# Performance work log

Hardware: AMD Instinct MI355X
Metric: run time of the kernel (lower is better)

The kernel has to match this reference:

```python
import jax, jax.numpy as jnp
import numpy as np

B, C, T, H, NCLS = 512, 22, 1000, 64, 4


def setup_inputs() -> dict:
    key = jax.random.key(0)
    ks = jax.random.split(key, 8)
    s_ih = 1.0 / np.sqrt(H)
    x = jax.random.normal(ks[0], (B, C, T), dtype=jnp.float32)
    # PyTorch LSTM params: gate order [i, f, g, o], each of size H
    W_ih = jax.random.uniform(ks[1], (4 * H, C), minval=-s_ih, maxval=s_ih, dtype=jnp.float32)
    W_hh = jax.random.uniform(ks[2], (4 * H, H), minval=-s_ih, maxval=s_ih, dtype=jnp.float32)
    b_ih = jax.random.uniform(ks[3], (4 * H,), minval=-s_ih, maxval=s_ih, dtype=jnp.float32)
    b_hh = jax.random.uniform(ks[4], (4 * H,), minval=-s_ih, maxval=s_ih, dtype=jnp.float32)
    s_fc = 1.0 / np.sqrt(H * T)
    W_fc = jax.random.uniform(ks[5], (NCLS, H * T), minval=-s_fc, maxval=s_fc, dtype=jnp.float32)
    b_fc = jax.random.uniform(ks[6], (NCLS,), minval=-s_fc, maxval=s_fc, dtype=jnp.float32)
    return {"x": x, "W_ih": W_ih, "W_hh": W_hh, "b_ih": b_ih, "b_hh": b_hh,
            "W_fc": W_fc, "b_fc": b_fc}


def _lstm(xs, W_ih, W_hh, b_ih, b_hh):
    # xs: [B, T, C] -> outputs [B, T, H]
    b = xs.shape[0]
    # precompute input projections for all timesteps: [T, B, 4H]
    x_proj = jnp.einsum('btc,gc->tbg', xs, W_ih) + (b_ih + b_hh)
    h0 = jnp.zeros((b, W_hh.shape[1]), xs.dtype)
    c0 = jnp.zeros_like(h0)

    def step(carry, xp):
        h, c = carry
        gates = xp + h @ W_hh.T  # [B, 4H]
        i, f, g, o = jnp.split(gates, 4, axis=-1)
        i = jax.nn.sigmoid(i)
        f = jax.nn.sigmoid(f)
        g = jnp.tanh(g)
        o = jax.nn.sigmoid(o)
        c = f * c + i * g
        h = o * jnp.tanh(c)
        return (h, c), h

    _, hs = jax.lax.scan(step, (h0, c0), x_proj)  # hs: [T, B, H]
    return jnp.transpose(hs, (1, 0, 2))  # [B, T, H]


def reference(x, W_ih, W_hh, b_ih, b_hh, W_fc, b_fc):
    xs = jnp.transpose(x, (0, 2, 1))  # [B, T, C]  (permute(0,2,1))
    hs = _lstm(xs, W_ih, W_hh, b_ih, b_hh)  # [B, T, H]
    flat = hs.reshape(hs.shape[0], -1)  # [B, T*H], time-major per row
    logits = flat @ W_fc.T + b_fc  # [B, 4]
    return jax.nn.softmax(logits, axis=1)
```

## Files before the change

### kernel.cpp

```cpp
#include <hip/hip_runtime.h>

#define BB   512
#define CC   22
#define TT   1000
#define HH   64
#define NCLS 4
#define TC   250
#define NCHUNK (TT / TC)
#define XROW 12

typedef _Float16 f16;
typedef __attribute__((ext_vector_type(2))) _Float16 h2;

__device__ __forceinline__ float sigm(float x) {
    return 1.0f / (1.0f + __expf(-x));
}
__device__ __forceinline__ float tanh_(float x) {
    float e = __expf(-2.0f * fabsf(x));
    float r = (1.0f - e) / (1.0f + e);
    return copysignf(r, x);
}

__device__ __forceinline__ h2 u2h(unsigned u) {
    union { unsigned u; h2 h; } c; c.u = u; return c.h;
}
__device__ __forceinline__ unsigned h2u(h2 h) {
    union { unsigned u; h2 h; } c; c.h = h; return c.u;
}

__global__ __launch_bounds__(64, 1) void lstm_wave(
    const float* __restrict__ x,
    const float* __restrict__ W_ih,
    const float* __restrict__ W_hh,
    const float* __restrict__ b_ih,
    const float* __restrict__ b_hh,
    const float* __restrict__ W_fc,
    const float* __restrict__ b_fc,
    float* __restrict__ out)
{
    __shared__ __align__(16) h2  xs[TC][XROW];
    __shared__ __align__(16) f16 hbuf[HH];

    const int lane = threadIdx.x;
    const int r    = blockIdx.x;

    unsigned whh[4][32];
    unsigned wih[4][11];
    float bias[4];
    #pragma unroll
    for (int g = 0; g < 4; ++g) {
        const int row = g * HH + lane;
        const float* wr = W_hh + row * HH;
        #pragma unroll
        for (int k = 0; k < 32; ++k)
            whh[g][k] = h2u(h2{(f16)wr[2 * k], (f16)wr[2 * k + 1]});
        const float* wi = W_ih + row * CC;
        #pragma unroll
        for (int k = 0; k < 11; ++k)
            wih[g][k] = h2u(h2{(f16)wi[2 * k], (f16)wi[2 * k + 1]});
        bias[g] = b_ih[row] + b_hh[row];
    }
    #pragma unroll
    for (int g = 0; g < 4; ++g) {
        #pragma unroll
        for (int k = 0; k < 32; ++k) asm volatile("" : "+v"(whh[g][k]));
        #pragma unroll
        for (int k = 0; k < 11; ++k) asm volatile("" : "+v"(wih[g][k]));
        asm volatile("" : "+v"(bias[g]));
    }

    hbuf[lane] = (f16)0.0f;
    float c = 0.0f;
    float fc0 = 0.f, fc1 = 0.f, fc2 = 0.f, fc3 = 0.f;
    const float* p0 = W_fc + 0 * (TT * HH) + lane;
    const float* p1 = W_fc + 1 * (TT * HH) + lane;
    const float* p2 = W_fc + 2 * (TT * HH) + lane;
    const float* p3 = W_fc + 3 * (TT * HH) + lane;
    const float* xrow = x + (size_t)r * (CC * TT);

    for (int chunk = 0; chunk < NCHUNK; ++chunk) {
        for (int tb = 0; tb < TC; tb += 64) {
            const int t = tb + lane;
            if (t < TC) {
                const float* gx = xrow + chunk * TC + t;
                union { h2 h[XROW]; uint4 q[3]; } U;
                #pragma unroll
                for (int k = 0; k < 11; ++k)
                    U.h[k] = h2{(f16)gx[(2 * k) * TT], (f16)gx[(2 * k + 1) * TT]};
                U.h[11] = h2{(f16)0.0f, (f16)0.0f};
                uint4* dst = (uint4*)&xs[t][0];
                dst[0] = U.q[0]; dst[1] = U.q[1]; dst[2] = U.q[2];
            }
        }

        for (int tt = 0; tt < TC; ++tt) {
            union { uint4 q[8]; h2 h[32]; } H;
            const uint4* hr = (const uint4*)hbuf;
            #pragma unroll
            for (int i = 0; i < 8; ++i) H.q[i] = hr[i];

            union { uint4 q[3]; h2 h[XROW]; } X;
            const uint4* xr = (const uint4*)&xs[tt][0];
            X.q[0] = xr[0]; X.q[1] = xr[1]; X.q[2] = xr[2];

            float w0 = *p0, w1 = *p1, w2 = *p2, w3 = *p3;
            p0 += HH; p1 += HH; p2 += HH; p3 += HH;

            float a0 = bias[0], a1 = bias[1], a2 = bias[2], a3 = bias[3];
            #pragma unroll
            for (int k = 0; k < 11; ++k) {
                a0 = __builtin_amdgcn_fdot2(X.h[k], u2h(wih[0][k]), a0, false);
                a1 = __builtin_amdgcn_fdot2(X.h[k], u2h(wih[1][k]), a1, false);
                a2 = __builtin_amdgcn_fdot2(X.h[k], u2h(wih[2][k]), a2, false);
                a3 = __builtin_amdgcn_fdot2(X.h[k], u2h(wih[3][k]), a3, false);
            }
            #pragma unroll
            for (int k = 0; k < 32; ++k) {
                a0 = __builtin_amdgcn_fdot2(H.h[k], u2h(whh[0][k]), a0, false);
                a1 = __builtin_amdgcn_fdot2(H.h[k], u2h(whh[1][k]), a1, false);
                a2 = __builtin_amdgcn_fdot2(H.h[k], u2h(whh[2][k]), a2, false);
                a3 = __builtin_amdgcn_fdot2(H.h[k], u2h(whh[3][k]), a3, false);
            }

            float iv = sigm(a0), fv = sigm(a1), gv = tanh_(a2), ov = sigm(a3);
            c = fv * c + iv * gv;
            float h = ov * tanh_(c);

            fc0 += h * w0; fc1 += h * w1; fc2 += h * w2; fc3 += h * w3;

            hbuf[lane] = (f16)h;
        }
    }

    #pragma unroll
    for (int off = 32; off; off >>= 1) {
        fc0 += __shfl_down(fc0, off);
        fc1 += __shfl_down(fc1, off);
        fc2 += __shfl_down(fc2, off);
        fc3 += __shfl_down(fc3, off);
    }
    if (lane == 0) {
        float l0 = fc0 + b_fc[0], l1 = fc1 + b_fc[1];
        float l2 = fc2 + b_fc[2], l3 = fc3 + b_fc[3];
        float m  = fmaxf(fmaxf(l0, l1), fmaxf(l2, l3));
        float e0 = __expf(l0 - m), e1 = __expf(l1 - m);
        float e2 = __expf(l2 - m), e3 = __expf(l3 - m);
        float s  = e0 + e1 + e2 + e3;
        float4 o; o.x = e0 / s; o.y = e1 / s; o.z = e2 / s; o.w = e3 / s;
        *(float4*)(out + r * NCLS) = o;
    }
}

extern "C" void kernel_launch(void* const* d_in, const int* in_sizes, int n_in,
                              void* d_out, int out_size, void* d_ws, size_t ws_size,
                              hipStream_t stream) {
    const float* x    = (const float*)d_in[0];
    const float* W_ih = (const float*)d_in[1];
    const float* W_hh = (const float*)d_in[2];
    const float* b_ih = (const float*)d_in[3];
    const float* b_hh = (const float*)d_in[4];
    const float* W_fc = (const float*)d_in[5];
    const float* b_fc = (const float*)d_in[6];
    float* out = (float*)d_out;

    lstm_wave<<<BB, 64, 0, stream>>>(x, W_ih, W_hh, b_ih, b_hh, W_fc, b_fc, out);
}
```

Baseline: 681.1 us.

## Split LSTM gate dot products across two waves with per-step LDS reduction

Each block now runs two waves. Each wave holds half of the recurrent and input weight columns and computes partial gate sums over its half of h and x. The partial sums are swapped through a double-buffered shared array with a barrier every timestep, which roughly halves the serial fdot2 chain per step. The price is a workgroup barrier and an LDS round trip inside the recurrence. Divisions in sigmoid, tanh and softmax are also replaced with hardware reciprocal approximations.

```diff
diff --git a/kernel.cpp b/kernel.cpp
--- a/kernel.cpp
+++ b/kernel.cpp
@@ -7,17 +7,18 @@
 #define NCLS 4
 #define TC   250
 #define NCHUNK (TT / TC)
-#define XROW 12
+#define XSL  16
 
 typedef _Float16 f16;
 typedef __attribute__((ext_vector_type(2))) _Float16 h2;
 
 __device__ __forceinline__ float sigm(float x) {
-    return 1.0f / (1.0f + __expf(-x));
+    float e = __expf(-x);
+    return __builtin_amdgcn_rcpf(1.0f + e);
 }
 __device__ __forceinline__ float tanh_(float x) {
     float e = __expf(-2.0f * fabsf(x));
-    float r = (1.0f - e) / (1.0f + e);
+    float r = (1.0f - e) * __builtin_amdgcn_rcpf(1.0f + e);
     return copysignf(r, x);
 }
 
@@ -28,7 +29,7 @@
     union { unsigned u; h2 h; } c; c.h = h; return c.u;
 }
 
-__global__ __launch_bounds__(64, 1) void lstm_wave(
+__global__ __launch_bounds__(128, 1) void lstm_wave2(
     const float* __restrict__ x,
     const float* __restrict__ W_ih,
     const float* __restrict__ W_hh,
@@ -38,95 +39,120 @@
     const float* __restrict__ b_fc,
     float* __restrict__ out)
 {
-    __shared__ __align__(16) h2  xs[TC][XROW];
-    __shared__ __align__(16) f16 hbuf[HH];
+    __shared__ __align__(16) h2    xs[TC][XSL];
+    __shared__ __align__(16) f16   hbuf[HH];
+    __shared__ __align__(16) float part[2][2][HH][4];
+    __shared__ float tmp4[NCLS];
 
-    const int lane = threadIdx.x;
+    const int tid  = threadIdx.x;
+    const int w    = tid >> 6;
+    const int lane = tid & 63;
     const int r    = blockIdx.x;
 
-    unsigned whh[4][32];
-    unsigned wih[4][11];
-    float bias[4];
+    unsigned whh[4][16];
+    unsigned wih[4][6];
+    float    bias[4];
     #pragma unroll
     for (int g = 0; g < 4; ++g) {
         const int row = g * HH + lane;
-        const float* wr = W_hh + row * HH;
+        const float* wr = W_hh + row * HH + 32 * w;
         #pragma unroll
-        for (int k = 0; k < 32; ++k)
+        for (int k = 0; k < 16; ++k)
             whh[g][k] = h2u(h2{(f16)wr[2 * k], (f16)wr[2 * k + 1]});
-        const float* wi = W_ih + row * CC;
+        const float* wi = W_ih + row * CC + 12 * w;
         #pragma unroll
-        for (int k = 0; k < 11; ++k)
-            wih[g][k] = h2u(h2{(f16)wi[2 * k], (f16)wi[2 * k + 1]});
-        bias[g] = b_ih[row] + b_hh[row];
+        for (int k = 0; k < 6; ++k) {
+            unsigned v = 0u;
+            if (w == 0 || k < 5)
+                v = h2u(h2{(f16)wi[2 * k], (f16)wi[2 * k + 1]});
+            wih[g][k] = v;
+        }
+        bias[g] = (w == 0) ? (b_ih[row] + b_hh[row]) : 0.0f;
     }
     #pragma unroll
     for (int g = 0; g < 4; ++g) {
         #pragma unroll
-        for (int k = 0; k < 32; ++k) asm volatile("" : "+v"(whh[g][k]));
+        for (int k = 0; k < 16; ++k) asm volatile("" : "+v"(whh[g][k]));
         #pragma unroll
-        for (int k = 0; k < 11; ++k) asm volatile("" : "+v"(wih[g][k]));
+        for (int k = 0; k < 6; ++k)  asm volatile("" : "+v"(wih[g][k]));
         asm volatile("" : "+v"(bias[g]));
     }
 
     hbuf[lane] = (f16)0.0f;
     float c = 0.0f;
-    float fc0 = 0.f, fc1 = 0.f, fc2 = 0.f, fc3 = 0.f;
-    const float* p0 = W_fc + 0 * (TT * HH) + lane;
-    const float* p1 = W_fc + 1 * (TT * HH) + lane;
-    const float* p2 = W_fc + 2 * (TT * HH) + lane;
-    const float* p3 = W_fc + 3 * (TT * HH) + lane;
+    float fca = 0.0f, fcb = 0.0f;
+    const float* pa = W_fc + (size_t)(2 * w)     * (TT * HH) + lane;
+    const float* pb = W_fc + (size_t)(2 * w + 1) * (TT * HH) + lane;
     const float* xrow = x + (size_t)r * (CC * TT);
 
     for (int chunk = 0; chunk < NCHUNK; ++chunk) {
-        for (int tb = 0; tb < TC; tb += 64) {
-            const int t = tb + lane;
+        for (int tb = 0; tb < TC; tb += 128) {
+            const int t = tb + tid;
             if (t < TC) {
                 const float* gx = xrow + chunk * TC + t;
-                union { h2 h[XROW]; uint4 q[3]; } U;
+                union { h2 h[XSL]; uint4 q[4]; } U;
                 #pragma unroll
-                for (int k = 0; k < 11; ++k)
+                for (int k = 0; k < 6; ++k)
                     U.h[k] = h2{(f16)gx[(2 * k) * TT], (f16)gx[(2 * k + 1) * TT]};
-                U.h[11] = h2{(f16)0.0f, (f16)0.0f};
+                U.h[6] = h2{(f16)0.0f, (f16)0.0f};
+                U.h[7] = h2{(f16)0.0f, (f16)0.0f};
+                #pragma unroll
+                for (int j = 0; j < 5; ++j)
+                    U.h[8 + j] = h2{(f16)gx[(12 + 2 * j) * TT], (f16)gx[(13 + 2 * j) * TT]};
+                U.h[13] = h2{(f16)0.0f, (f16)0.0f};
+                U.h[14] = h2{(f16)0.0f, (f16)0.0f};
+                U.h[15] = h2{(f16)0.0f, (f16)0.0f};
                 uint4* dst = (uint4*)&xs[t][0];
-                dst[0] = U.q[0]; dst[1] = U.q[1]; dst[2] = U.q[2];
+                dst[0] = U.q[0]; dst[1] = U.q[1]; dst[2] = U.q[2]; dst[3] = U.q[3];
             }
         }
+        __syncthreads();
 
         for (int tt = 0; tt < TC; ++tt) {
-            union { uint4 q[8]; h2 h[32]; } H;
-            const uint4* hr = (const uint4*)hbuf;
+            float wa = *pa, wb = *pb;
+            pa += HH; pb += HH;
+
+            union { uint4 q[4]; h2 h[16]; } H;
+            const uint4* hr = (const uint4*)(hbuf + 32 * w);
             #pragma unroll
-            for (int i = 0; i < 8; ++i) H.q[i] = hr[i];
+            for (int i = 0; i < 4; ++i) H.q[i] = hr[i];
 
-            union { uint4 q[3]; h2 h[XROW]; } X;
-            const uint4* xr = (const uint4*)&xs[tt][0];
-            X.q[0] = xr[0]; X.q[1] = xr[1]; X.q[2] = xr[2];
-
-            float w0 = *p0, w1 = *p1, w2 = *p2, w3 = *p3;
-            p0 += HH; p1 += HH; p2 += HH; p3 += HH;
+            __align__(16) h2 X[6];
+            {
+                const h2* xp = &xs[tt][8 * w];
+                *(uint4*)&X[0] = *(const uint4*)xp;
+                *(uint2*)&X[4] = *(const uint2*)(xp + 4);
+            }
 
             float a0 = bias[0], a1 = bias[1], a2 = bias[2], a3 = bias[3];
             #pragma unroll
-            for (int k = 0; k < 11; ++k) {
-                a0 = __builtin_amdgcn_fdot2(X.h[k], u2h(wih[0][k]), a0, false);
-                a1 = __builtin_amdgcn_fdot2(X.h[k], u2h(wih[1][k]), a1, false);
-                a2 = __builtin_amdgcn_fdot2(X.h[k], u2h(wih[2][k]), a2, false);
-                a3 = __builtin_amdgcn_fdot2(X.h[k], u2h(wih[3][k]), a3, false);
+            for (int k = 0; k < 6; ++k) {
+                a0 = __builtin_amdgcn_fdot2(X[k], u2h(wih[0][k]), a0, false);
+                a1 = __builtin_amdgcn_fdot2(X[k], u2h(wih[1][k]), a1, false);
+                a2 = __builtin_amdgcn_fdot2(X[k], u2h(wih[2][k]), a2, false);
+                a3 = __builtin_amdgcn_fdot2(X[k], u2h(wih[3][k]), a3, false);
             }
             #pragma unroll
-            for (int k = 0; k < 32; ++k) {
+            for (int k = 0; k < 16; ++k) {
                 a0 = __builtin_amdgcn_fdot2(H.h[k], u2h(whh[0][k]), a0, false);
                 a1 = __builtin_amdgcn_fdot2(H.h[k], u2h(whh[1][k]), a1, false);
                 a2 = __builtin_amdgcn_fdot2(H.h[k], u2h(whh[2][k]), a2, false);
                 a3 = __builtin_amdgcn_fdot2(H.h[k], u2h(whh[3][k]), a3, false);
             }
 
+            const int buf = tt & 1;
+            float4 mine; mine.x = a0; mine.y = a1; mine.z = a2; mine.w = a3;
+            *(float4*)&part[buf][w][lane][0] = mine;
+            __syncthreads();
+            float4 oth = *(const float4*)&part[buf][1 - w][lane][0];
+            a0 += oth.x; a1 += oth.y; a2 += oth.z; a3 += oth.w;
+
             float iv = sigm(a0), fv = sigm(a1), gv = tanh_(a2), ov = sigm(a3);
             c = fv * c + iv * gv;
             float h = ov * tanh_(c);
 
-            fc0 += h * w0; fc1 += h * w1; fc2 += h * w2; fc3 += h * w3;
+            fca += h * wa;
+            fcb += h * wb;
 
             hbuf[lane] = (f16)h;
         }
@@ -134,19 +160,21 @@
 
     #pragma unroll
     for (int off = 32; off; off >>= 1) {
-        fc0 += __shfl_down(fc0, off);
-        fc1 += __shfl_down(fc1, off);
-        fc2 += __shfl_down(fc2, off);
-        fc3 += __shfl_down(fc3, off);
+        fca += __shfl_down(fca, off);
+        fcb += __shfl_down(fcb, off);
     }
     if (lane == 0) {
-        float l0 = fc0 + b_fc[0], l1 = fc1 + b_fc[1];
-        float l2 = fc2 + b_fc[2], l3 = fc3 + b_fc[3];
+        tmp4[2 * w]     = fca + b_fc[2 * w];
+        tmp4[2 * w + 1] = fcb + b_fc[2 * w + 1];
+    }
+    __syncthreads();
+    if (tid == 0) {
+        float l0 = tmp4[0], l1 = tmp4[1], l2 = tmp4[2], l3 = tmp4[3];
         float m  = fmaxf(fmaxf(l0, l1), fmaxf(l2, l3));
         float e0 = __expf(l0 - m), e1 = __expf(l1 - m);
         float e2 = __expf(l2 - m), e3 = __expf(l3 - m);
-        float s  = e0 + e1 + e2 + e3;
-        float4 o; o.x = e0 / s; o.y = e1 / s; o.z = e2 / s; o.w = e3 / s;
+        float is = __builtin_amdgcn_rcpf(e0 + e1 + e2 + e3);
+        float4 o; o.x = e0 * is; o.y = e1 * is; o.z = e2 * is; o.w = e3 * is;
         *(float4*)(out + r * NCLS) = o;
     }
 }
@@ -163,5 +191,5 @@
     const float* b_fc = (const float*)d_in[6];
     float* out = (float*)d_out;
 
-    lstm_wave<<<BB, 64, 0, stream>>>(x, W_ih, W_hh, b_ih, b_hh, W_fc, b_fc, out);
+    lstm_wave2<<<BB, 128, 0, stream>>>(x, W_ih, W_hh, b_ih, b_hh, W_fc, b_fc, out);
 }
```

Measured after the change: 708.9 us. +4.1%, slower.

## Process two batch rows per wave sharing register weights; use rcp for activations

Applied to the files above, without the earlier changes.

Each single-wave block now runs the LSTM recurrence for two batch rows, reusing the register-resident weight fragments and the per-step W_fc loads, and halving the grid. The two independent recurrences give instruction-level parallelism to hide LDS and transcendental latency. Divisions in sigmoid, tanh and softmax are replaced by hardware reciprocal approximations. The trade-off is fewer waves across the GPU, so the per-wave serial work doubles while CU-level parallelism drops.

```diff
diff --git a/kernel.cpp b/kernel.cpp
--- a/kernel.cpp
+++ b/kernel.cpp
@@ -13,11 +13,12 @@
 typedef __attribute__((ext_vector_type(2))) _Float16 h2;
 
 __device__ __forceinline__ float sigm(float x) {
-    return 1.0f / (1.0f + __expf(-x));
+    float e = __expf(-x);
+    return __builtin_amdgcn_rcpf(1.0f + e);
 }
 __device__ __forceinline__ float tanh_(float x) {
     float e = __expf(-2.0f * fabsf(x));
-    float r = (1.0f - e) / (1.0f + e);
+    float r = (1.0f - e) * __builtin_amdgcn_rcpf(1.0f + e);
     return copysignf(r, x);
 }
 
@@ -28,7 +29,7 @@
     union { unsigned u; h2 h; } c; c.h = h; return c.u;
 }
 
-__global__ __launch_bounds__(64, 1) void lstm_wave(
+__global__ __launch_bounds__(64, 1) void lstm_2row(
     const float* __restrict__ x,
     const float* __restrict__ W_ih,
     const float* __restrict__ W_hh,
@@ -38,11 +39,14 @@
     const float* __restrict__ b_fc,
     float* __restrict__ out)
 {
-    __shared__ __align__(16) h2  xs[TC][XROW];
-    __shared__ __align__(16) f16 hbuf[HH];
+    __shared__ __align__(16) h2  xsA[TC][XROW];
+    __shared__ __align__(16) h2  xsB[TC][XROW];
+    __shared__ __align__(16) f16 hbA[HH];
+    __shared__ __align__(16) f16 hbB[HH];
 
     const int lane = threadIdx.x;
-    const int r    = blockIdx.x;
+    const int rA   = blockIdx.x * 2;
+    const int rB   = rA + 1;
 
     unsigned whh[4][32];
     unsigned wih[4][11];
@@ -69,85 +73,123 @@
         asm volatile("" : "+v"(bias[g]));
     }
 
-    hbuf[lane] = (f16)0.0f;
-    float c = 0.0f;
-    float fc0 = 0.f, fc1 = 0.f, fc2 = 0.f, fc3 = 0.f;
+    hbA[lane] = (f16)0.0f;
+    hbB[lane] = (f16)0.0f;
+    float cA = 0.0f, cB = 0.0f;
+    float fa0 = 0.f, fa1 = 0.f, fa2 = 0.f, fa3 = 0.f;
+    float fb0 = 0.f, fb1 = 0.f, fb2 = 0.f, fb3 = 0.f;
     const float* p0 = W_fc + 0 * (TT * HH) + lane;
     const float* p1 = W_fc + 1 * (TT * HH) + lane;
     const float* p2 = W_fc + 2 * (TT * HH) + lane;
     const float* p3 = W_fc + 3 * (TT * HH) + lane;
-    const float* xrow = x + (size_t)r * (CC * TT);
+    const float* xrowA = x + (size_t)rA * (CC * TT);
+    const float* xrowB = x + (size_t)rB * (CC * TT);
 
     for (int chunk = 0; chunk < NCHUNK; ++chunk) {
         for (int tb = 0; tb < TC; tb += 64) {
             const int t = tb + lane;
             if (t < TC) {
-                const float* gx = xrow + chunk * TC + t;
-                union { h2 h[XROW]; uint4 q[3]; } U;
+                const float* gA = xrowA + chunk * TC + t;
+                const float* gB = xrowB + chunk * TC + t;
+                union { h2 h[XROW]; uint4 q[3]; } UA, UB;
                 #pragma unroll
-                for (int k = 0; k < 11; ++k)
-                    U.h[k] = h2{(f16)gx[(2 * k) * TT], (f16)gx[(2 * k + 1) * TT]};
-                U.h[11] = h2{(f16)0.0f, (f16)0.0f};
-                uint4* dst = (uint4*)&xs[t][0];
-                dst[0] = U.q[0]; dst[1] = U.q[1]; dst[2] = U.q[2];
+                for (int k = 0; k < 11; ++k) {
+                    UA.h[k] = h2{(f16)gA[(2 * k) * TT], (f16)gA[(2 * k + 1) * TT]};
+                    UB.h[k] = h2{(f16)gB[(2 * k) * TT], (f16)gB[(2 * k + 1) * TT]};
+                }
+                UA.h[11] = h2{(f16)0.0f, (f16)0.0f};
+                UB.h[11] = h2{(f16)0.0f, (f16)0.0f};
+                uint4* dA = (uint4*)&xsA[t][0];
+                uint4* dB = (uint4*)&xsB[t][0];
+                dA[0] = UA.q[0]; dA[1] = UA.q[1]; dA[2] = UA.q[2];
+                dB[0] = UB.q[0]; dB[1] = UB.q[1]; dB[2] = UB.q[2];
             }
         }
 
         for (int tt = 0; tt < TC; ++tt) {
-            union { uint4 q[8]; h2 h[32]; } H;
-            const uint4* hr = (const uint4*)hbuf;
-            #pragma unroll
-            for (int i = 0; i < 8; ++i) H.q[i] = hr[i];
-
-            union { uint4 q[3]; h2 h[XROW]; } X;
-            const uint4* xr = (const uint4*)&xs[tt][0];
-            X.q[0] = xr[0]; X.q[1] = xr[1]; X.q[2] = xr[2];
-
             float w0 = *p0, w1 = *p1, w2 = *p2, w3 = *p3;
             p0 += HH; p1 += HH; p2 += HH; p3 += HH;
 
-            float a0 = bias[0], a1 = bias[1], a2 = bias[2], a3 = bias[3];
+            union { uint4 q[8]; h2 h[32]; } HA, HB;
+            const uint4* ha = (const uint4*)hbA;
+            const uint4* hb = (const uint4*)hbB;
+            #pragma unroll
+            for (int i = 0; i < 8; ++i) { HA.q[i] = ha[i]; HB.q[i] = hb[i]; }
+
+            union { uint4 q[3]; h2 h[XROW]; } XA, XB;
+            const uint4* xa = (const uint4*)&xsA[tt][0];
+            const uint4* xb = (const uint4*)&xsB[tt][0];
+            XA.q[0] = xa[0]; XA.q[1] = xa[1]; XA.q[2] = xa[2];
+            XB.q[0] = xb[0]; XB.q[1] = xb[1]; XB.q[2] = xb[2];
+
+            float aA0 = bias[0], aA1 = bias[1], aA2 = bias[2], aA3 = bias[3];
+            float aB0 = bias[0], aB1 = bias[1], aB2 = bias[2], aB3 = bias[3];
             #pragma unroll
             for (int k = 0; k < 11; ++k) {
-                a0 = __builtin_amdgcn_fdot2(X.h[k], u2h(wih[0][k]), a0, false);
-                a1 = __builtin_amdgcn_fdot2(X.h[k], u2h(wih[1][k]), a1, false);
-                a2 = __builtin_amdgcn_fdot2(X.h[k], u2h(wih[2][k]), a2, false);
-                a3 = __builtin_amdgcn_fdot2(X.h[k], u2h(wih[3][k]), a3, false);
+                aA0 = __builtin_amdgcn_fdot2(XA.h[k], u2h(wih[0][k]), aA0, false);
+                aB0 = __builtin_amdgcn_fdot2(XB.h[k], u2h(wih[0][k]), aB0, false);
+                aA1 = __builtin_amdgcn_fdot2(XA.h[k], u2h(wih[1][k]), aA1, false);
+                aB1 = __builtin_amdgcn_fdot2(XB.h[k], u2h(wih[1][k]), aB1, false);
+                aA2 = __builtin_amdgcn_fdot2(XA.h[k], u2h(wih[2][k]), aA2, false);
+                aB2 = __builtin_amdgcn_fdot2(XB.h[k], u2h(wih[2][k]), aB2, false);
+                aA3 = __builtin_amdgcn_fdot2(XA.h[k], u2h(wih[3][k]), aA3, false);
+                aB3 = __builtin_amdgcn_fdot2(XB.h[k], u2h(wih[3][k]), aB3, false);
             }
             #pragma unroll
             for (int k = 0; k < 32; ++k) {
-                a0 = __builtin_amdgcn_fdot2(H.h[k], u2h(whh[0][k]), a0, false);
-                a1 = __builtin_amdgcn_fdot2(H.h[k], u2h(whh[1][k]), a1, false);
-                a2 = __builtin_amdgcn_fdot2(H.h[k], u2h(whh[2][k]), a2, false);
-                a3 = __builtin_amdgcn_fdot2(H.h[k], u2h(whh[3][k]), a3, false);
+                aA0 = __builtin_amdgcn_fdot2(HA.h[k], u2h(whh[0][k]), aA0, false);
+                aB0 = __builtin_amdgcn_fdot2(HB.h[k], u2h(whh[0][k]), aB0, false);
+                aA1 = __builtin_amdgcn_fdot2(HA.h[k], u2h(whh[1][k]), aA1, false);
+                aB1 = __builtin_amdgcn_fdot2(HB.h[k], u2h(whh[1][k]), aB1, false);
+                aA2 = __builtin_amdgcn_fdot2(HA.h[k], u2h(whh[2][k]), aA2, false);
+                aB2 = __builtin_amdgcn_fdot2(HB.h[k], u2h(whh[2][k]), aB2, false);
+                aA3 = __builtin_amdgcn_fdot2(HA.h[k], u2h(whh[3][k]), aA3, false);
+                aB3 = __builtin_amdgcn_fdot2(HB.h[k], u2h(whh[3][k]), aB3, false);
             }
 
-            float iv = sigm(a0), fv = sigm(a1), gv = tanh_(a2), ov = sigm(a3);
-            c = fv * c + iv * gv;
-            float h = ov * tanh_(c);
-
-            fc0 += h * w0; fc1 += h * w1; fc2 += h * w2; fc3 += h * w3;
-
-            hbuf[lane] = (f16)h;
+            float iA = sigm(aA0), fA = sigm(aA1), gA = tanh_(aA2), oA = sigm(aA3);
+            float iB = sigm(aB0), fB = sigm(aB1), gB = tanh_(aB2), oB = sigm(aB3);
+            cA = fA * cA + iA * gA;
+            cB = fB * cB + iB * gB;
+            float hA = oA * tanh_(cA);
+            float hB = oB * tanh_(cB);
+
+            fa0 += hA * w0; fa1 += hA * w1; fa2 += hA * w2; fa3 += hA * w3;
+            fb0 += hB * w0; fb1 += hB * w1; fb2 += hB * w2; fb3 += hB * w3;
+
+            hbA[lane] = (f16)hA;
+            hbB[lane] = (f16)hB;
         }
     }
 
     #pragma unroll
     for (int off = 32; off; off >>= 1) {
-        fc0 += __shfl_down(fc0, off);
-        fc1 += __shfl_down(fc1, off);
-        fc2 += __shfl_down(fc2, off);
-        fc3 += __shfl_down(fc3, off);
+        fa0 += __shfl_down(fa0, off); fa1 += __shfl_down(fa1, off);
+        fa2 += __shfl_down(fa2, off); fa3 += __shfl_down(fa3, off);
+        fb0 += __shfl_down(fb0, off); fb1 += __shfl_down(fb1, off);
+        fb2 += __shfl_down(fb2, off); fb3 += __shfl_down(fb3, off);
     }
     if (lane == 0) {
-        float l0 = fc0 + b_fc[0], l1 = fc1 + b_fc[1];
-        float l2 = fc2 + b_fc[2], l3 = fc3 + b_fc[3];
-        float m  = fmaxf(fmaxf(l0, l1), fmaxf(l2, l3));
-        float e0 = __expf(l0 - m), e1 = __expf(l1 - m);
-        float e2 = __expf(l2 - m), e3 = __expf(l3 - m);
-        float s  = e0 + e1 + e2 + e3;
-        float4 o; o.x = e0 / s; o.y = e1 / s; o.z = e2 / s; o.w = e3 / s;
-        *(float4*)(out + r * NCLS) = o;
+        {
+            float l0 = fa0 + b_fc[0], l1 = fa1 + b_fc[1];
+            float l2 = fa2 + b_fc[2], l3 = fa3 + b_fc[3];
+            float m  = fmaxf(fmaxf(l0, l1), fmaxf(l2, l3));
+            float e0 = __expf(l0 - m), e1 = __expf(l1 - m);
+            float e2 = __expf(l2 - m), e3 = __expf(l3 - m);
+            float is = __builtin_amdgcn_rcpf(e0 + e1 + e2 + e3);
+            float4 o; o.x = e0 * is; o.y = e1 * is; o.z = e2 * is; o.w = e3 * is;
+            *(float4*)(out + rA * NCLS) = o;
+        }
+        {
+            float l0 = fb0 + b_fc[0], l1 = fb1 + b_fc[1];
+            float l2 = fb2 + b_fc[2], l3 = fb3 + b_fc[3];
+            float m  = fmaxf(fmaxf(l0, l1), fmaxf(l2, l3));
+            float e0 = __expf(l0 - m), e1 = __expf(l1 - m);
+            float e2 = __expf(l2 - m), e3 = __expf(l3 - m);
+            float is = __builtin_amdgcn_rcpf(e0 + e1 + e2 + e3);
+            float4 o; o.x = e0 * is; o.y = e1 * is; o.z = e2 * is; o.w = e3 * is;
+            *(float4*)(out + rB * NCLS) = o;
+        }
     }
 }
 
@@ -163,5 +205,5 @@
     const float* b_fc = (const float*)d_in[6];
     float* out = (float*)d_out;
 
-    lstm_wave<<<BB, 64, 0, stream>>>(x, W_ih, W_hh, b_ih, b_hh, W_fc, b_fc, out);
-}
+    lstm_2row<<<BB / 2, 64, 0, stream>>>(x, W_ih, W_hh, b_ih, b_hh, W_fc, b_fc, out);
+}
```

Result: slower. 1.007 ms (+47.8%).

## Precompute LSTM input projections in a separate kernel, streamed from workspace

Applied to the files above, without the earlier changes.

Adds a parallel xproj kernel that computes W_ih·x plus biases for every batch and timestep and stores them as fp16 in the workspace, gate-interleaved per hidden unit. The recurrent kernel then loads one 8-byte value per lane per step instead of doing 44 input dot products, and no longer needs the shared-memory staging of x. Divisions in the activations and softmax are replaced with hardware reciprocal approximations. In exchange it adds about 262 MB of workspace traffic, a second launch and an extra fp16 rounding of the projection; the old fused kernel stays as a fallback when the workspace is too small.

```diff
diff --git a/kernel.cpp b/kernel.cpp
--- a/kernel.cpp
+++ b/kernel.cpp
@@ -5,22 +5,21 @@
 #define TT   1000
 #define HH   64
 #define NCLS 4
-#define TC   250
-#define NCHUNK (TT / TC)
-#define XROW 12
+#define FCW  (TT * HH)
+#define TB   100
 
 typedef _Float16 f16;
 typedef __attribute__((ext_vector_type(2))) _Float16 h2;
 
 __device__ __forceinline__ float sigm(float x) {
-    return 1.0f / (1.0f + __expf(-x));
+    float e = __expf(-x);
+    return __builtin_amdgcn_rcpf(1.0f + e);
 }
 __device__ __forceinline__ float tanh_(float x) {
     float e = __expf(-2.0f * fabsf(x));
-    float r = (1.0f - e) / (1.0f + e);
+    float r = (1.0f - e) * __builtin_amdgcn_rcpf(1.0f + e);
     return copysignf(r, x);
 }
-
 __device__ __forceinline__ h2 u2h(unsigned u) {
     union { unsigned u; h2 h; } c; c.u = u; return c.h;
 }
@@ -28,16 +27,146 @@
     union { unsigned u; h2 h; } c; c.h = h; return c.u;
 }
 
-__global__ __launch_bounds__(64, 1) void lstm_wave(
+__global__ __launch_bounds__(256) void xproj(
     const float* __restrict__ x,
     const float* __restrict__ W_ih,
-    const float* __restrict__ W_hh,
     const float* __restrict__ b_ih,
     const float* __restrict__ b_hh,
+    f16* __restrict__ xp)
+{
+    __shared__ __align__(16) float xt[CC][TB];
+
+    const int tid = threadIdx.x;
+    const int t0  = blockIdx.x * TB;
+    const int b   = blockIdx.y;
+    const int hid = tid >> 2;
+    const int g   = tid & 3;
+    const int row = g * HH + hid;
+
+    for (int s = tid; s < CC * TB; s += 256) {
+        const int c = s / TB, t = s - c * TB;
+        xt[c][t] = x[((size_t)b * CC + c) * TT + t0 + t];
+    }
+    float wr[CC];
+    #pragma unroll
+    for (int c = 0; c < CC; ++c) wr[c] = W_ih[row * CC + c];
+    const float bias = b_ih[row] + b_hh[row];
+    __syncthreads();
+
+    f16* op = xp + ((size_t)b * TT + t0) * 256 + tid;
+    for (int t = 0; t < TB; t += 4) {
+        float a0 = bias, a1 = bias, a2 = bias, a3 = bias;
+        #pragma unroll
+        for (int c = 0; c < CC; ++c) {
+            const float4 xv = *(const float4*)&xt[c][t];
+            a0 += wr[c] * xv.x; a1 += wr[c] * xv.y;
+            a2 += wr[c] * xv.z; a3 += wr[c] * xv.w;
+        }
+        op[0]   = (f16)a0;
+        op[256] = (f16)a1;
+        op[512] = (f16)a2;
+        op[768] = (f16)a3;
+        op += 1024;
+    }
+}
+
+__global__ __attribute__((amdgpu_waves_per_eu(1, 1)))
+__launch_bounds__(64) void lstm_rec(
+    const uint2* __restrict__ xp,
+    const float* __restrict__ W_hh,
     const float* __restrict__ W_fc,
     const float* __restrict__ b_fc,
     float* __restrict__ out)
 {
+    __shared__ __align__(16) f16 hbuf[HH];
+
+    const int lane = threadIdx.x;
+    const int r    = blockIdx.x;
+
+    unsigned whh[4][32];
+    #pragma unroll
+    for (int g = 0; g < 4; ++g) {
+        const float* wr = W_hh + (g * HH + lane) * HH;
+        #pragma unroll
+        for (int k = 0; k < 32; ++k)
+            whh[g][k] = h2u(h2{(f16)wr[2 * k], (f16)wr[2 * k + 1]});
+    }
+    #pragma unroll
+    for (int g = 0; g < 4; ++g)
+        #pragma unroll
+        for (int k = 0; k < 32; ++k) asm volatile("" : "+v"(whh[g][k]));
+
+    hbuf[lane] = (f16)0.0f;
+    float c = 0.0f;
+    float fc0 = 0.f, fc1 = 0.f, fc2 = 0.f, fc3 = 0.f;
+    const uint2* px = xp + (size_t)r * TT * HH + lane;
+    const float* p0 = W_fc + 0 * FCW + lane;
+    const float* p1 = W_fc + 1 * FCW + lane;
+    const float* p2 = W_fc + 2 * FCW + lane;
+    const float* p3 = W_fc + 3 * FCW + lane;
+
+    for (int t = 0; t < TT; ++t) {
+        const uint2 xv = px[(size_t)t * HH];
+        const float w0 = *p0, w1 = *p1, w2 = *p2, w3 = *p3;
+        p0 += HH; p1 += HH; p2 += HH; p3 += HH;
+
+        union { uint4 q[8]; h2 h[32]; } H;
+        const uint4* hr = (const uint4*)hbuf;
+        #pragma unroll
+        for (int i = 0; i < 8; ++i) H.q[i] = hr[i];
+
+        float a0 = 0.f, a1 = 0.f, a2 = 0.f, a3 = 0.f;
+        #pragma unroll
+        for (int k = 0; k < 32; ++k) {
+            a0 = __builtin_amdgcn_fdot2(H.h[k], u2h(whh[0][k]), a0, false);
+            a1 = __builtin_amdgcn_fdot2(H.h[k], u2h(whh[1][k]), a1, false);
+            a2 = __builtin_amdgcn_fdot2(H.h[k], u2h(whh[2][k]), a2, false);
+            a3 = __builtin_amdgcn_fdot2(H.h[k], u2h(whh[3][k]), a3, false);
+        }
+        const h2 pif = u2h(xv.x), pgo = u2h(xv.y);
+        a0 += (float)pif[0]; a1 += (float)pif[1];
+        a2 += (float)pgo[0]; a3 += (float)pgo[1];
+
+        const float iv = sigm(a0), fv = sigm(a1);
+        const float gv = tanh_(a2), ov = sigm(a3);
+        c = fv * c + iv * gv;
+        const float h = ov * tanh_(c);
+
+        fc0 += h * w0; fc1 += h * w1; fc2 += h * w2; fc3 += h * w3;
+
+        hbuf[lane] = (f16)h;
+    }
+
+    #pragma unroll
+    for (int off = 32; off; off >>= 1) {
+        fc0 += __shfl_down(fc0, off);
+        fc1 += __shfl_down(fc1, off);
+        fc2 += __shfl_down(fc2, off);
+        fc3 += __shfl_down(fc3, off);
+    }
+    if (lane == 0) {
+        const float l0 = fc0 + b_fc[0], l1 = fc1 + b_fc[1];
+        const float l2 = fc2 + b_fc[2], l3 = fc3 + b_fc[3];
+        const float m  = fmaxf(fmaxf(l0, l1), fmaxf(l2, l3));
+        const float e0 = __expf(l0 - m), e1 = __expf(l1 - m);
+        const float e2 = __expf(l2 - m), e3 = __expf(l3 - m);
+        const float is = __builtin_amdgcn_rcpf(e0 + e1 + e2 + e3);
+        float4 o; o.x = e0 * is; o.y = e1 * is; o.z = e2 * is; o.w = e3 * is;
+        *(float4*)(out + r * NCLS) = o;
+    }
+}
+
+#define TC   250
+#define NCHUNK (TT / TC)
+#define XROW 12
+
+__global__ __attribute__((amdgpu_waves_per_eu(1, 1)))
+__launch_bounds__(64) void lstm_fb(
+    const float* __restrict__ x, const float* __restrict__ W_ih,
+    const float* __restrict__ W_hh, const float* __restrict__ b_ih,
+    const float* __restrict__ b_hh, const float* __restrict__ W_fc,
+    const float* __restrict__ b_fc, float* __restrict__ out)
+{
     __shared__ __align__(16) h2  xs[TC][XROW];
     __shared__ __align__(16) f16 hbuf[HH];
 
@@ -72,10 +201,10 @@
     hbuf[lane] = (f16)0.0f;
     float c = 0.0f;
     float fc0 = 0.f, fc1 = 0.f, fc2 = 0.f, fc3 = 0.f;
-    const float* p0 = W_fc + 0 * (TT * HH) + lane;
-    const float* p1 = W_fc + 1 * (TT * HH) + lane;
-    const float* p2 = W_fc + 2 * (TT * HH) + lane;
-    const float* p3 = W_fc + 3 * (TT * HH) + lane;
+    const float* p0 = W_fc + 0 * FCW + lane;
+    const float* p1 = W_fc + 1 * FCW + lane;
+    const float* p2 = W_fc + 2 * FCW + lane;
+    const float* p3 = W_fc + 3 * FCW + lane;
     const float* xrow = x + (size_t)r * (CC * TT);
 
     for (int chunk = 0; chunk < NCHUNK; ++chunk) {
@@ -92,20 +221,16 @@
                 dst[0] = U.q[0]; dst[1] = U.q[1]; dst[2] = U.q[2];
             }
         }
-
         for (int tt = 0; tt < TC; ++tt) {
             union { uint4 q[8]; h2 h[32]; } H;
             const uint4* hr = (const uint4*)hbuf;
             #pragma unroll
             for (int i = 0; i < 8; ++i) H.q[i] = hr[i];
-
             union { uint4 q[3]; h2 h[XROW]; } X;
             const uint4* xr = (const uint4*)&xs[tt][0];
             X.q[0] = xr[0]; X.q[1] = xr[1]; X.q[2] = xr[2];
-
             float w0 = *p0, w1 = *p1, w2 = *p2, w3 = *p3;
             p0 += HH; p1 += HH; p2 += HH; p3 += HH;
-
             float a0 = bias[0], a1 = bias[1], a2 = bias[2], a3 = bias[3];
             #pragma unroll
             for (int k = 0; k < 11; ++k) {
@@ -121,17 +246,14 @@
                 a2 = __builtin_amdgcn_fdot2(H.h[k], u2h(whh[2][k]), a2, false);
                 a3 = __builtin_amdgcn_fdot2(H.h[k], u2h(whh[3][k]), a3, false);
             }
-
-            float iv = sigm(a0), fv = sigm(a1), gv = tanh_(a2), ov = sigm(a3);
+            const float iv = sigm(a0), fv = sigm(a1);
+            const float gv = tanh_(a2), ov = sigm(a3);
             c = fv * c + iv * gv;
-            float h = ov * tanh_(c);
-
+            const float h = ov * tanh_(c);
             fc0 += h * w0; fc1 += h * w1; fc2 += h * w2; fc3 += h * w3;
-
             hbuf[lane] = (f16)h;
         }
     }
-
     #pragma unroll
     for (int off = 32; off; off >>= 1) {
         fc0 += __shfl_down(fc0, off);
@@ -140,13 +262,13 @@
         fc3 += __shfl_down(fc3, off);
     }
     if (lane == 0) {
-        float l0 = fc0 + b_fc[0], l1 = fc1 + b_fc[1];
-        float l2 = fc2 + b_fc[2], l3 = fc3 + b_fc[3];
-        float m  = fmaxf(fmaxf(l0, l1), fmaxf(l2, l3));
-        float e0 = __expf(l0 - m), e1 = __expf(l1 - m);
-        float e2 = __expf(l2 - m), e3 = __expf(l3 - m);
-        float s  = e0 + e1 + e2 + e3;
-        float4 o; o.x = e0 / s; o.y = e1 / s; o.z = e2 / s; o.w = e3 / s;
+        const float l0 = fc0 + b_fc[0], l1 = fc1 + b_fc[1];
+        const float l2 = fc2 + b_fc[2], l3 = fc3 + b_fc[3];
+        const float m  = fmaxf(fmaxf(l0, l1), fmaxf(l2, l3));
+        const float e0 = __expf(l0 - m), e1 = __expf(l1 - m);
+        const float e2 = __expf(l2 - m), e3 = __expf(l3 - m);
+        const float is = __builtin_amdgcn_rcpf(e0 + e1 + e2 + e3);
+        float4 o; o.x = e0 * is; o.y = e1 * is; o.z = e2 * is; o.w = e3 * is;
         *(float4*)(out + r * NCLS) = o;
     }
 }
@@ -163,5 +285,12 @@
     const float* b_fc = (const float*)d_in[6];
     float* out = (float*)d_out;
 
-    lstm_wave<<<BB, 64, 0, stream>>>(x, W_ih, W_hh, b_ih, b_hh, W_fc, b_fc, out);
-}
+    const size_t need = (size_t)BB * TT * HH * 4 * sizeof(f16);
+    if (d_ws != nullptr && ws_size >= need) {
+        f16* xp = (f16*)d_ws;
+        xproj<<<dim3(TT / TB, BB), 256, 0, stream>>>(x, W_ih, b_ih, b_hh, xp);
+        lstm_rec<<<BB, 64, 0, stream>>>((const uint2*)xp, W_hh, W_fc, b_fc, out);
+    } else {
+        lstm_fb<<<BB, 64, 0, stream>>>(x, W_ih, W_hh, b_ih, b_hh, W_fc, b_fc, out);
+    }
+}
```

New measurement: 729.5 us. 1.07x slower.
